# Kernel tuning notes

Measured on AMD Instinct MI355X. Metric: run time of the kernel, lower is better.

The kernel has to match this reference:

```python
import jax, jax.numpy as jnp
import numpy as np

N_NODES = 50000
N_EDGES = 800000
H = 64  # n_hid


def _linear_params(key, fan_in, fan_out):
    lim = 1.0 / np.sqrt(fan_in)
    kw, kb = jax.random.split(key)
    w = jax.random.uniform(kw, (fan_in, fan_out), minval=-lim, maxval=lim, dtype=jnp.float32)
    b = jax.random.uniform(kb, (fan_out,), minval=-lim, maxval=lim, dtype=jnp.float32)
    return w, b


def setup_inputs() -> dict:
    key = jax.random.key(0)
    ks = jax.random.split(key, 10)
    nf_gc = jax.random.normal(ks[0], (N_NODES, H), dtype=jnp.float32)
    src = jax.random.randint(ks[1], (N_EDGES,), 0, N_NODES, dtype=jnp.int32)
    dst = jax.random.randint(ks[2], (N_EDGES,), 0, N_NODES, dtype=jnp.int32)
    res_w1, res_b1 = _linear_params(ks[3], H, H)
    res_w2, res_b2 = _linear_params(ks[4], H, H)
    lin1_w, lin1_b = _linear_params(ks[5], H, H)
    lin2_w, lin2_b = _linear_params(ks[6], H, H)
    msg_w1, msg_b1 = _linear_params(ks[7], 2 * H, 2 * H)
    msg_w2, msg_b2 = _linear_params(ks[8], 2 * H, 2 * H + 1)
    red_w, red_b = _linear_params(ks[9], 3 * H, H)
    return {
        'nf_gc': nf_gc, 'src': src, 'dst': dst,
        'res_w1': res_w1, 'res_b1': res_b1, 'res_w2': res_w2, 'res_b2': res_b2,
        'lin1_w': lin1_w, 'lin1_b': lin1_b, 'lin2_w': lin2_w, 'lin2_b': lin2_b,
        'msg_w1': msg_w1, 'msg_b1': msg_b1, 'msg_w2': msg_w2, 'msg_b2': msg_b2,
        'red_w': red_w, 'red_b': red_b,
    }


def reference(nf_gc, src, dst, res_w1, res_b1, res_w2, res_b2,
              lin1_w, lin1_b, lin2_w, lin2_b,
              msg_w1, msg_b1, msg_w2, msg_b2, red_w, red_b):
    n = nf_gc.shape[0]
    h = lin1_w.shape[0]
    # Residual block: lin2(lin1(x)) + x (no activation)
    x = ((nf_gc @ res_w1 + res_b1) @ res_w2 + res_b2) + nf_gc
    x1 = x @ lin1_w + lin1_b
    # Edge message: concat(src feat, dst feat) -> MLP(2h -> 2h -> 2h+1)
    e = jnp.concatenate([x[src], x[dst]], axis=1)          # [E, 2h]
    hmid = jax.nn.leaky_relu(e @ msg_w1 + msg_b1, 0.2)     # [E, 2h]
    o = hmid @ msg_w2 + msg_b2                             # [E, 2h+1]
    k = jax.nn.sigmoid(o[:, :1])
    f1 = o[:, 1:1 + h] * k
    f2 = o[:, 1 + h:] * k
    # Scatter-reduce: sum for f1, max for f2 (DGL gives 0 for isolated nodes)
    nfoc1 = jax.ops.segment_sum(f1, dst, num_segments=n)
    neg_inf = jnp.array(-jnp.inf, dtype=f2.dtype)
    nfoc2 = jnp.full((n, h), neg_inf, dtype=f2.dtype).at[dst].max(f2)
    deg = jnp.zeros((n,), dtype=f2.dtype).at[dst].add(1.0)
    nfoc2 = jnp.where(deg[:, None] > 0, nfoc2, 0.0)
    # Node reduce MLP (single linear 3h -> h), then outer lin2
    new_x = jnp.concatenate([x, nfoc1, nfoc2], axis=1) @ red_w + red_b
    x2 = new_x @ lin2_w + lin2_b
    return x1 + x2
```

## Files before the change

### kernel.cpp

```cpp
#include <hip/hip_runtime.h>

#define NN 50000
#define NE 800000

typedef _Float16 half8 __attribute__((ext_vector_type(8)));
typedef _Float16 half4 __attribute__((ext_vector_type(4)));
typedef float f32x4 __attribute__((ext_vector_type(4)));
typedef unsigned long long u64;

static const size_t XHOFF  = 0;
static const size_t POFF   = 3200000;
static const size_t QOFF   = 6400000;
static const size_t N1OFF  = 9600000;
static const size_t N2OFF  = 12800000;
static const size_t W2TOFF = 16000000;
static const size_t WGHOFF = 16008192;
static const size_t RW1HOFF= 16008256;
static const size_t RW2HOFF= 16010304;
static const size_t L1WHOFF= 16012352;
static const size_t PWHOFF = 16014400;
static const size_t QWHOFF = 16018496;
static const size_t CNTOFF = 16022592;
static const size_t CUROFF = 16072592;
static const size_t PARTOFF= 16122592;
static const size_t SDOFF  = 16122848;
static const size_t FWOFF  = 17722848;
static const size_t FBOFF  = 17729200;

__device__ __forceinline__ unsigned fenc(float f){
  unsigned b = __float_as_uint(f);
  return (b & 0x80000000u) ? ~b : (b | 0x80000000u);
}
__device__ __forceinline__ float fdec(unsigned u){
  return (u & 0x80000000u) ? __uint_as_float(u & 0x7fffffffu) : __uint_as_float(~u);
}

__device__ __forceinline__ int kperm(int kp){
  const int kg = kp >> 5, rem = kp & 31, kt = rem >> 2, j = rem & 3;
  return kt*16 + kg*4 + j;
}

__global__ __launch_bounds__(256) void prep_k(
    const float* __restrict__ w2, const float* __restrict__ rw1,
    const float* __restrict__ rw2, const float* __restrict__ l1w,
    const float* __restrict__ mw1,
    const float* __restrict__ redw, const float* __restrict__ redb,
    const float* __restrict__ l2w, const float* __restrict__ l2b,
    _Float16* __restrict__ w2t, _Float16* __restrict__ w2gh,
    _Float16* __restrict__ rw1h, _Float16* __restrict__ rw2h,
    _Float16* __restrict__ l1wh, _Float16* __restrict__ pwh,
    _Float16* __restrict__ qwh,
    _Float16* __restrict__ fwh, float* __restrict__ fb,
    const int* __restrict__ dst, unsigned* __restrict__ counts)
{
  __shared__ float sl2[64][8];
  const int b = blockIdx.x;
  if (b < 177){
    int i = b * 256 + threadIdx.x;
    if (i < 16384){
      int c = i >> 7, kp = i & 127;
      w2t[i] = (_Float16)w2[kperm(kp)*129 + 1 + c];
    } else if (i < 16512){
      int kp = i - 16384;
      w2gh[kp] = (_Float16)w2[kperm(kp)*129];
    } else if (i < 20608){
      int idx = i - 16512, c = idx >> 6, k = idx & 63;
      rw1h[idx] = (_Float16)rw1[k*64 + c];
    } else if (i < 24704){
      int idx = i - 20608, c = idx >> 6, k = idx & 63;
      rw2h[idx] = (_Float16)rw2[k*64 + c];
    } else if (i < 28800){
      int idx = i - 24704, c = idx >> 6, k = idx & 63;
      l1wh[idx] = (_Float16)l1w[k*64 + c];
    } else if (i < 36992){
      int idx = i - 28800, c = idx >> 6, k = idx & 63;
      pwh[idx] = (_Float16)mw1[k*128 + c];
    } else if (i < 45184){
      int idx = i - 36992, c = idx >> 6, k = idx & 63;
      qwh[idx] = (_Float16)mw1[(64 + k)*128 + c];
    }
  } else if (b < 185){
    const int b2 = b - 177;
    const int c0 = b2 * 8;
    const int t = threadIdx.x;
    #pragma unroll
    for (int i = 0; i < 2; ++i){
      int idx = t + i*256;
      int j = idx >> 3, cc = idx & 7;
      sl2[j][cc] = l2w[j*64 + c0 + cc];
    }
    __syncthreads();
    for (int o = t; o < 1536; o += 256){
      int k = o >> 3, cc = o & 7;
      const float4* rw = (const float4*)&redw[k*64];
      float a = 0.f;
      #pragma unroll
      for (int q = 0; q < 16; ++q){
        const float4 r4 = rw[q];
        a = fmaf(r4.x, sl2[q*4+0][cc], a);
        a = fmaf(r4.y, sl2[q*4+1][cc], a);
        a = fmaf(r4.z, sl2[q*4+2][cc], a);
        a = fmaf(r4.w, sl2[q*4+3][cc], a);
      }
      fwh[(size_t)(c0 + cc)*192 + k] = (_Float16)a;
    }
    if (t < 8){
      float a = l2b[c0 + t];
      #pragma unroll 8
      for (int j = 0; j < 64; ++j) a = fmaf(redb[j], sl2[j][t], a);
      fb[c0 + t] = a;
    }
  } else {
    int e = (b - 185) * 256 + threadIdx.x;
    if (e < NE) atomicAdd(&counts[dst[e]], 1u);
  }
}

__global__ __launch_bounds__(256) void scanA2(const unsigned* __restrict__ counts,
                                              unsigned* __restrict__ partial,
                                              uint4* __restrict__ nfz)
{
  __shared__ unsigned s[256];
  const int b = blockIdx.x;
  const int t = threadIdx.x;
  if (b < 196){
    const int idx = b * 256 + t;
    s[t] = (idx < NN) ? counts[idx] : 0u;
    __syncthreads();
    for (int d = 128; d > 0; d >>= 1){
      if (t < d) s[t] += s[t + d];
      __syncthreads();
    }
    if (t == 0) partial[b] = s[0];
  } else {
    const size_t i0 = ((size_t)(b - 196) * 256 + t) * 4;
    #pragma unroll
    for (int i = 0; i < 4; ++i){
      const size_t idx = i0 + i;
      if (idx < 1600000) nfz[idx] = make_uint4(0u,0u,0u,0u);
    }
  }
}

__global__ __launch_bounds__(256) void scanC2(const unsigned* __restrict__ counts,
                                              const unsigned* __restrict__ partial,
                                              unsigned* __restrict__ cursor)
{
  __shared__ unsigned sp[256];
  __shared__ unsigned s[256];
  const int t = threadIdx.x;
  const int b = blockIdx.x;
  sp[t] = (t < 196 && t < b) ? partial[t] : 0u;
  __syncthreads();
  for (int d = 128; d > 0; d >>= 1){
    if (t < d) sp[t] += sp[t + d];
    __syncthreads();
  }
  const unsigned boff = sp[0];
  const int idx = b * 256 + t;
  unsigned v = (idx < NN) ? counts[idx] : 0u;
  s[t] = v;
  __syncthreads();
  for (int d = 1; d < 256; d <<= 1){
    unsigned u = (t >= d) ? s[t - d] : 0u;
    __syncthreads();
    s[t] += u;
    __syncthreads();
  }
  if (idx < NN) cursor[idx] = boff + s[t] - v;
}

__global__ __launch_bounds__(256) void combo_k(
    const int* __restrict__ src, const int* __restrict__ dst,
    unsigned* __restrict__ cursor, u64* __restrict__ sdbuf,
    const float* __restrict__ nf,
    const _Float16* __restrict__ rw1h, const float* __restrict__ rb1,
    const _Float16* __restrict__ rw2h, const float* __restrict__ rb2,
    const _Float16* __restrict__ l1wh, const float* __restrict__ l1b,
    const _Float16* __restrict__ pwh, const _Float16* __restrict__ qwh,
    const float* __restrict__ mb1,
    _Float16* __restrict__ xh, _Float16* __restrict__ Pp, _Float16* __restrict__ Qp,
    float* __restrict__ out)
{
  __shared__ _Float16 sM[64][72];
  __shared__ _Float16 sT[64][72];
  const int b = blockIdx.x;
  const int t = threadIdx.x;

  if (b < 3125){
    int e = b * 256 + t;
    if (e < NE){
      const int d = dst[e];
      unsigned slot = atomicAdd(&cursor[d], 1u);
      sdbuf[slot] = ((u64)(unsigned)d << 32) | (unsigned)src[e];
    }
    return;
  }

  const int lane = t & 63, wv = t >> 6;
  const int l15 = lane & 15, kg = lane >> 4;
  const int n0 = (b - 3125) * 64;

  {
    const int rr = t >> 4, c4 = (t & 15) * 4;
    #pragma unroll
    for (int i = 0; i < 4; ++i){
      int r = rr + i*16, n = n0 + r;
      float4 v = make_float4(0.f,0.f,0.f,0.f);
      if (n < NN) v = *(const float4*)&nf[(size_t)n*64 + c4];
      half4 h; h[0]=(_Float16)v.x; h[1]=(_Float16)v.y; h[2]=(_Float16)v.z; h[3]=(_Float16)v.w;
      *(half4*)&sM[r][c4] = h;
    }
  }
  __syncthreads();

  const int col = wv*16 + l15;

  {
    half4 bf[4];
    #pragma unroll
    for (int kt = 0; kt < 4; ++kt) bf[kt] = *(const half4*)&rw1h[col*64 + kt*16 + kg*4];
    const float bias = rb1[col];
    #pragma unroll
    for (int rt = 0; rt < 4; ++rt){
      f32x4 acc = {0.f,0.f,0.f,0.f};
      #pragma unroll
      for (int kt = 0; kt < 4; ++kt){
        const half4 af = *(const half4*)&sM[rt*16 + l15][kt*16 + kg*4];
        acc = __builtin_amdgcn_mfma_f32_16x16x16f16(af, bf[kt], acc, 0, 0, 0);
      }
      #pragma unroll
      for (int reg = 0; reg < 4; ++reg)
        sT[rt*16 + kg*4 + reg][col] = (_Float16)(acc[reg] + bias);
    }
  }
  __syncthreads();

  {
    half4 bf[4];
    #pragma unroll
    for (int kt = 0; kt < 4; ++kt) bf[kt] = *(const half4*)&rw2h[col*64 + kt*16 + kg*4];
    const float bias = rb2[col];
    #pragma unroll
    for (int rt = 0; rt < 4; ++rt){
      f32x4 acc = {0.f,0.f,0.f,0.f};
      #pragma unroll
      for (int kt = 0; kt < 4; ++kt){
        const half4 af = *(const half4*)&sT[rt*16 + l15][kt*16 + kg*4];
        acc = __builtin_amdgcn_mfma_f32_16x16x16f16(af, bf[kt], acc, 0, 0, 0);
      }
      #pragma unroll
      for (int reg = 0; reg < 4; ++reg){
        const int row = rt*16 + kg*4 + reg;
        const float xv = acc[reg] + bias + (float)sM[row][col];
        const _Float16 xvh = (_Float16)xv;
        const int n = n0 + row;
        if (n < NN) xh[(size_t)n*64 + col] = xvh;
        sM[row][col] = xvh;
      }
    }
  }
  __syncthreads();

  {
    half4 bf[4];
    #pragma unroll
    for (int kt = 0; kt < 4; ++kt) bf[kt] = *(const half4*)&l1wh[col*64 + kt*16 + kg*4];
    const float bias = l1b[col];
    #pragma unroll
    for (int rt = 0; rt < 4; ++rt){
      f32x4 acc = {0.f,0.f,0.f,0.f};
      #pragma unroll
      for (int kt = 0; kt < 4; ++kt){
        const half4 af = *(const half4*)&sM[rt*16 + l15][kt*16 + kg*4];
        acc = __builtin_amdgcn_mfma_f32_16x16x16f16(af, bf[kt], acc, 0, 0, 0);
      }
      #pragma unroll
      for (int reg = 0; reg < 4; ++reg){
        const int row = rt*16 + kg*4 + reg;
        const int n = n0 + row;
        if (n < NN) out[(size_t)n*64 + col] = acc[reg] + bias;
      }
    }
  }

  #pragma unroll
  for (int g = 0; g < 2; ++g){
    const _Float16* WH = g ? qwh : pwh;
    _Float16* dstp = g ? Qp : Pp;
    #pragma unroll
    for (int h = 0; h < 2; ++h){
      const int ct = h*4 + wv;
      const int colp = ct*16 + l15;
      half4 bf[4];
      #pragma unroll
      for (int kt = 0; kt < 4; ++kt) bf[kt] = *(const half4*)&WH[colp*64 + kt*16 + kg*4];
      const float bias = g ? 0.f : mb1[colp];
      const int kgc = l15 >> 2, jj = l15 & 3;
      const int pos = kgc*32 + ct*4 + jj;
      #pragma unroll
      for (int rt = 0; rt < 4; ++rt){
        f32x4 acc = {0.f,0.f,0.f,0.f};
        #pragma unroll
        for (int kt = 0; kt < 4; ++kt){
          const half4 af = *(const half4*)&sM[rt*16 + l15][kt*16 + kg*4];
          acc = __builtin_amdgcn_mfma_f32_16x16x16f16(af, bf[kt], acc, 0, 0, 0);
        }
        #pragma unroll
        for (int reg = 0; reg < 4; ++reg){
          const int row = rt*16 + kg*4 + reg;
          const int n = n0 + row;
          if (n < NN) dstp[(size_t)n*128 + pos] = (_Float16)(acc[reg] + bias);
        }
      }
    }
  }
}

__global__ __launch_bounds__(256) void edge_mlp8(
    const u64* __restrict__ sd,
    const _Float16* __restrict__ Pp, const _Float16* __restrict__ Qp,
    const _Float16* __restrict__ w2t, const _Float16* __restrict__ w2gh,
    const float* __restrict__ b2,
    float* __restrict__ nfoc1, unsigned* __restrict__ nfoc2)
{
  __shared__ _Float16 sA[64][136];
  __shared__ _Float16 sOutH[64][136];
  __shared__ float sK[2][64];
  __shared__ int   sD[2][64];
  const int t = threadIdx.x;
  const int lane = t & 63, wv = t >> 6;
  const int r  = lane & 15;
  const int kg = lane >> 4;
  const int row0 = wv * 16;
  const int base = blockIdx.x * 256;

  const int ct0 = wv * 2;
  half4 bf0[8], bf1[8];
  half8 wgr[4];
  float bias0, bias1;
  {
    const int col0 = ct0*16 + r, col1 = (ct0+1)*16 + r;
    bias0 = b2[1 + col0]; bias1 = b2[1 + col1];
    const _Float16* w0p = &w2t[(size_t)col0*128 + kg*32];
    const _Float16* w1p = &w2t[(size_t)col1*128 + kg*32];
    #pragma unroll
    for (int kt = 0; kt < 8; ++kt){
      bf0[kt] = *(const half4*)&w0p[kt*4];
      bf1[kt] = *(const half4*)&w1p[kt*4];
    }
    #pragma unroll
    for (int i = 0; i < 4; ++i) wgr[i] = *(const half8*)&w2gh[kg*32 + i*8];
  }
  const float gb = b2[0];

#define LOADRAW(PH, QH, SS, DD, TILE) { \
    const u64 sdv = sd[base + (TILE)*64 + row0 + r]; \
    SS = (int)(unsigned)(sdv & 0xffffffffu); \
    DD = (int)(unsigned)(sdv >> 32); \
    const _Float16* pr = &Pp[(size_t)SS * 128 + kg*32]; \
    const _Float16* qr = &Qp[(size_t)DD * 128 + kg*32]; \
    PH[0] = *(const half8*)&pr[0];  PH[1] = *(const half8*)&pr[8]; \
    PH[2] = *(const half8*)&pr[16]; PH[3] = *(const half8*)&pr[24]; \
    QH[0] = *(const half8*)&qr[0];  QH[1] = *(const half8*)&qr[8]; \
    QH[2] = *(const half8*)&qr[16]; QH[3] = *(const half8*)&qr[24]; }

#define PROCESS(PH, QH, DD, BUF) { \
    if (kg == 0) sD[BUF][row0 + r] = DD; \
    float gp = 0.f; \
    _Pragma("unroll") \
    for (int i = 0; i < 4; ++i){ \
      half8 mv = PH[i] + QH[i]; \
      const half8 m2 = mv * (_Float16)0.2f; \
      mv = __builtin_elementwise_max(mv, m2); \
      _Pragma("unroll") \
      for (int j = 0; j < 8; ++j) \
        gp = fmaf((float)mv[j], (float)wgr[i][j], gp); \
      *(half8*)&sA[row0 + r][kg*32 + i*8] = mv; \
    } \
    gp += __shfl_xor(gp, 16); \
    gp += __shfl_xor(gp, 32); \
    if (kg == 0) sK[BUF][row0 + r] = 1.f / (1.f + expf(-(gp + gb))); }

#define COMPUTE() { \
    _Pragma("unroll") \
    for (int rt = 0; rt < 4; ++rt){ \
      half4 af[8]; \
      const _Float16* ar = &sA[rt*16 + r][kg*32]; \
      _Pragma("unroll") \
      for (int kt = 0; kt < 8; ++kt) af[kt] = *(const half4*)&ar[kt*4]; \
      f32x4 a0 = {0.f,0.f,0.f,0.f}, a1 = {0.f,0.f,0.f,0.f}; \
      _Pragma("unroll") \
      for (int kt = 0; kt < 8; ++kt){ \
        a0 = __builtin_amdgcn_mfma_f32_16x16x16f16(af[kt], bf0[kt], a0, 0, 0, 0); \
        a1 = __builtin_amdgcn_mfma_f32_16x16x16f16(af[kt], bf1[kt], a1, 0, 0, 0); \
      } \
      _Pragma("unroll") \
      for (int reg = 0; reg < 4; ++reg){ \
        const int row = rt*16 + kg*4 + reg; \
        sOutH[row][ ct0   *16 + r] = (_Float16)(a0[reg] + bias0); \
        sOutH[row][(ct0+1)*16 + r] = (_Float16)(a1[reg] + bias1); \
      } \
    } }

#define REDUCE(BUF) { \
    const int c = t & 127; \
    const int rbeg = (t >> 7) * 32; \
    const bool isSum = c < 64; \
    float acc = isSum ? 0.f : -1e30f; \
    int curd = sD[BUF][rbeg]; \
    _Pragma("unroll 4") \
    for (int rw = rbeg; rw < rbeg + 32; ++rw){ \
      const float v = (float)sOutH[rw][c] * sK[BUF][rw]; \
      acc = isSum ? (acc + v) : fmaxf(acc, v); \
      const bool last = (rw == rbeg + 31) || (sD[BUF][rw + 1] != curd); \
      if (last){ \
        if (isSum){ \
          unsafeAtomicAdd(&nfoc1[(size_t)curd*64 + c], acc); \
          acc = 0.f; \
        } else { \
          atomicMax(&nfoc2[(size_t)curd*64 + (c - 64)], fenc(acc)); \
          acc = -1e30f; \
        } \
        if (rw < rbeg + 31) curd = sD[BUF][rw + 1]; \
      } \
    } }

  int s0, d0, s1, d1;
  half8 ph0[4], qh0[4], ph1[4], qh1[4];

  LOADRAW(ph0, qh0, s0, d0, 0);

  LOADRAW(ph1, qh1, s1, d1, 1);
  PROCESS(ph0, qh0, d0, 0);
  __syncthreads();
  COMPUTE();
  __syncthreads();
  REDUCE(0);

  LOADRAW(ph0, qh0, s0, d0, 2);
  PROCESS(ph1, qh1, d1, 1);
  __syncthreads();
  COMPUTE();
  __syncthreads();
  REDUCE(1);

  LOADRAW(ph1, qh1, s1, d1, 3);
  PROCESS(ph0, qh0, d0, 0);
  __syncthreads();
  COMPUTE();
  __syncthreads();
  REDUCE(0);

  PROCESS(ph1, qh1, d1, 1);
  __syncthreads();
  COMPUTE();
  __syncthreads();
  REDUCE(1);

#undef LOADRAW
#undef PROCESS
#undef COMPUTE
#undef REDUCE
}

__global__ __launch_bounds__(256) void node_post_m(
    const _Float16* __restrict__ xh, const float* __restrict__ nfoc1,
    const unsigned* __restrict__ nfoc2, const unsigned* __restrict__ counts,
    const _Float16* __restrict__ fwh, const float* __restrict__ fb,
    float* __restrict__ out)
{
  __shared__ _Float16 sC[64][200];
  const int t = threadIdx.x;
  const int lane = t & 63, wv = t >> 6;
  const int l15 = lane & 15, kg = lane >> 4;
  const int n0 = blockIdx.x * 64;

  {
    const int rr = t >> 4, c4 = (t & 15) * 4;
    #pragma unroll
    for (int i = 0; i < 4; ++i){
      int r = rr + i*16, n = n0 + r;
      half4 xv = {};
      float4 f1 = make_float4(0,0,0,0);
      uint4 f2 = make_uint4(0,0,0,0);
      bool has = false;
      if (n < NN){
        xv = *(const half4*)&xh[(size_t)n*64 + c4];
        f1 = *(const float4*)&nfoc1[(size_t)n*64 + c4];
        f2 = *(const uint4*)&nfoc2[(size_t)n*64 + c4];
        has = counts[n] > 0u;
      }
      *(half4*)&sC[r][c4] = xv;
      half4 h1; h1[0]=(_Float16)f1.x; h1[1]=(_Float16)f1.y; h1[2]=(_Float16)f1.z; h1[3]=(_Float16)f1.w;
      *(half4*)&sC[r][64 + c4] = h1;
      half4 h2;
      h2[0] = has ? (_Float16)fdec(f2.x) : (_Float16)0.f;
      h2[1] = has ? (_Float16)fdec(f2.y) : (_Float16)0.f;
      h2[2] = has ? (_Float16)fdec(f2.z) : (_Float16)0.f;
      h2[3] = has ? (_Float16)fdec(f2.w) : (_Float16)0.f;
      *(half4*)&sC[r][128 + c4] = h2;
    }
  }
  __syncthreads();

  const int col = wv*16 + l15;
  half4 bf[12];
  #pragma unroll
  for (int kt = 0; kt < 12; ++kt) bf[kt] = *(const half4*)&fwh[col*192 + kt*16 + kg*4];
  const float bias = fb[col];

  #pragma unroll
  for (int rt = 0; rt < 4; ++rt){
    f32x4 acc = {0.f,0.f,0.f,0.f};
    #pragma unroll
    for (int kt = 0; kt < 12; ++kt){
      const half4 af = *(const half4*)&sC[rt*16 + l15][kt*16 + kg*4];
      acc = __builtin_amdgcn_mfma_f32_16x16x16f16(af, bf[kt], acc, 0, 0, 0);
    }
    #pragma unroll
    for (int reg = 0; reg < 4; ++reg){
      const int row = rt*16 + kg*4 + reg;
      const int n = n0 + row;
      if (n < NN) out[(size_t)n*64 + col] += acc[reg] + bias;
    }
  }
}

extern "C" void kernel_launch(void* const* d_in, const int* in_sizes, int n_in,
                              void* d_out, int out_size, void* d_ws, size_t ws_size,
                              hipStream_t stream)
{
  const float* nf   = (const float*)d_in[0];
  const int*   src  = (const int*)d_in[1];
  const int*   dst  = (const int*)d_in[2];
  const float* rw1  = (const float*)d_in[3];
  const float* rb1  = (const float*)d_in[4];
  const float* rw2  = (const float*)d_in[5];
  const float* rb2  = (const float*)d_in[6];
  const float* l1w  = (const float*)d_in[7];
  const float* l1b  = (const float*)d_in[8];
  const float* l2w  = (const float*)d_in[9];
  const float* l2b  = (const float*)d_in[10];
  const float* mw1  = (const float*)d_in[11];
  const float* mb1  = (const float*)d_in[12];
  const float* mw2  = (const float*)d_in[13];
  const float* mb2  = (const float*)d_in[14];
  const float* redw = (const float*)d_in[15];
  const float* redb = (const float*)d_in[16];

  float* ws = (float*)d_ws;
  _Float16*  xh     = (_Float16*)(ws + XHOFF);
  _Float16*  P      = (_Float16*)(ws + POFF);
  _Float16*  Q      = (_Float16*)(ws + QOFF);
  float*     nfoc1  = ws + N1OFF;
  unsigned*  nfoc2  = (unsigned*)(ws + N2OFF);
  _Float16*  w2t    = (_Float16*)(ws + W2TOFF);
  _Float16*  w2gh   = (_Float16*)(ws + WGHOFF);
  _Float16*  rw1h   = (_Float16*)(ws + RW1HOFF);
  _Float16*  rw2h   = (_Float16*)(ws + RW2HOFF);
  _Float16*  l1wh   = (_Float16*)(ws + L1WHOFF);
  _Float16*  pwh    = (_Float16*)(ws + PWHOFF);
  _Float16*  qwh    = (_Float16*)(ws + QWHOFF);
  unsigned*  counts = (unsigned*)(ws + CNTOFF);
  unsigned*  cursor = (unsigned*)(ws + CUROFF);
  unsigned*  partial= (unsigned*)(ws + PARTOFF);
  u64*       sdbuf  = (u64*)(ws + SDOFF);
  _Float16*  fwh    = (_Float16*)(ws + FWOFF);
  float*     fb     = ws + FBOFF;
  float*     out    = (float*)d_out;

  hipMemsetAsync(counts, 0, NN * sizeof(unsigned), stream);
  hipLaunchKernelGGL(prep_k, dim3(185 + 3125), dim3(256), 0, stream,
                     mw2, rw1, rw2, l1w, mw1, redw, redb, l2w, l2b,
                     w2t, w2gh, rw1h, rw2h, l1wh, pwh, qwh, fwh, fb, dst, counts);
  hipLaunchKernelGGL(scanA2, dim3(196 + 1563), dim3(256), 0, stream,
                     counts, partial, (uint4*)nfoc1);
  hipLaunchKernelGGL(scanC2, dim3(196), dim3(256), 0, stream, counts, partial, cursor);
  hipLaunchKernelGGL(combo_k, dim3(3125 + 782), dim3(256), 0, stream,
                     src, dst, cursor, sdbuf,
                     nf, rw1h, rb1, rw2h, rb2, l1wh, l1b, pwh, qwh, mb1,
                     xh, P, Q, out);
  hipLaunchKernelGGL(edge_mlp8, dim3(3125), dim3(256), 0, stream,
                     sdbuf, P, Q, w2t, w2gh, mb2, nfoc1, nfoc2);
  hipLaunchKernelGGL(node_post_m, dim3(782), dim3(256), 0, stream,
                     xh, nfoc1, nfoc2, counts, fwh, fb, out);
}
```

Before: 313.1 us.

## Split edge MLP output into sum/max halves and move zeroing into prep kernel

The edge MLP kernel now computes the f1 (sum) and f2 (max) output halves in two passes through a half-width shared buffer. The sum and max reductions become separate uniform loops with no per-row sum-or-max branch, and each thread handles 16 rows instead of 32. This reduces shared memory per block, which may allow more resident blocks, but adds two extra barriers per tile. Separately, zeroing of nfoc1 moves from the scan kernel into the prep kernel, so scanA only does the block partial sums.

```diff
diff --git a/kernel.cpp b/kernel.cpp
--- a/kernel.cpp
+++ b/kernel.cpp
@@ -51,6 +51,7 @@
     _Float16* __restrict__ l1wh, _Float16* __restrict__ pwh,
     _Float16* __restrict__ qwh,
     _Float16* __restrict__ fwh, float* __restrict__ fb,
+    uint4* __restrict__ nfz,
     const int* __restrict__ dst, unsigned* __restrict__ counts)
 {
   __shared__ float sl2[64][8];
@@ -110,36 +111,32 @@
       for (int j = 0; j < 64; ++j) a = fmaf(redb[j], sl2[j][t], a);
       fb[c0 + t] = a;
     }
-  } else {
-    int e = (b - 185) * 256 + threadIdx.x;
-    if (e < NE) atomicAdd(&counts[dst[e]], 1u);
-  }
-}
-
-__global__ __launch_bounds__(256) void scanA2(const unsigned* __restrict__ counts,
-                                              unsigned* __restrict__ partial,
-                                              uint4* __restrict__ nfz)
-{
-  __shared__ unsigned s[256];
-  const int b = blockIdx.x;
-  const int t = threadIdx.x;
-  if (b < 196){
-    const int idx = b * 256 + t;
-    s[t] = (idx < NN) ? counts[idx] : 0u;
-    __syncthreads();
-    for (int d = 128; d > 0; d >>= 1){
-      if (t < d) s[t] += s[t + d];
-      __syncthreads();
-    }
-    if (t == 0) partial[b] = s[0];
-  } else {
-    const size_t i0 = ((size_t)(b - 196) * 256 + t) * 4;
+  } else if (b < 1748){
+    const size_t i0 = ((size_t)(b - 185) * 256 + threadIdx.x) * 4;
     #pragma unroll
     for (int i = 0; i < 4; ++i){
       const size_t idx = i0 + i;
       if (idx < 1600000) nfz[idx] = make_uint4(0u,0u,0u,0u);
     }
-  }
+  } else {
+    int e = (b - 1748) * 256 + threadIdx.x;
+    if (e < NE) atomicAdd(&counts[dst[e]], 1u);
+  }
+}
+
+__global__ __launch_bounds__(256) void scanA(const unsigned* __restrict__ counts,
+                                             unsigned* __restrict__ partial)
+{
+  __shared__ unsigned s[256];
+  const int t = threadIdx.x;
+  const int idx = blockIdx.x * 256 + t;
+  s[t] = (idx < NN) ? counts[idx] : 0u;
+  __syncthreads();
+  for (int d = 128; d > 0; d >>= 1){
+    if (t < d) s[t] += s[t + d];
+    __syncthreads();
+  }
+  if (t == 0) partial[blockIdx.x] = s[0];
 }
 
 __global__ __launch_bounds__(256) void scanC2(const unsigned* __restrict__ counts,
@@ -317,7 +314,7 @@
   }
 }
 
-__global__ __launch_bounds__(256) void edge_mlp8(
+__global__ __launch_bounds__(256) void edge_mlp10(
     const u64* __restrict__ sd,
     const _Float16* __restrict__ Pp, const _Float16* __restrict__ Qp,
     const _Float16* __restrict__ w2t, const _Float16* __restrict__ w2gh,
@@ -325,7 +322,7 @@
     float* __restrict__ nfoc1, unsigned* __restrict__ nfoc2)
 {
   __shared__ _Float16 sA[64][136];
-  __shared__ _Float16 sOutH[64][136];
+  __shared__ _Float16 sOutHh[64][72];
   __shared__ float sK[2][64];
   __shared__ int   sD[2][64];
   const int t = threadIdx.x;
@@ -335,12 +332,11 @@
   const int row0 = wv * 16;
   const int base = blockIdx.x * 256;
 
-  const int ct0 = wv * 2;
   half4 bf0[8], bf1[8];
   half8 wgr[4];
   float bias0, bias1;
   {
-    const int col0 = ct0*16 + r, col1 = (ct0+1)*16 + r;
+    const int col0 = wv*16 + r, col1 = (wv+4)*16 + r;
     bias0 = b2[1 + col0]; bias1 = b2[1 + col1];
     const _Float16* w0p = &w2t[(size_t)col0*128 + kg*32];
     const _Float16* w1p = &w2t[(size_t)col1*128 + kg*32];
@@ -382,50 +378,66 @@
     gp += __shfl_xor(gp, 32); \
     if (kg == 0) sK[BUF][row0 + r] = 1.f / (1.f + expf(-(gp + gb))); }
 
-#define COMPUTE() { \
+#define COMPUTE_HALF(BF, BIAS) { \
     _Pragma("unroll") \
     for (int rt = 0; rt < 4; ++rt){ \
       half4 af[8]; \
       const _Float16* ar = &sA[rt*16 + r][kg*32]; \
       _Pragma("unroll") \
       for (int kt = 0; kt < 8; ++kt) af[kt] = *(const half4*)&ar[kt*4]; \
-      f32x4 a0 = {0.f,0.f,0.f,0.f}, a1 = {0.f,0.f,0.f,0.f}; \
+      f32x4 a0 = {0.f,0.f,0.f,0.f}; \
       _Pragma("unroll") \
-      for (int kt = 0; kt < 8; ++kt){ \
-        a0 = __builtin_amdgcn_mfma_f32_16x16x16f16(af[kt], bf0[kt], a0, 0, 0, 0); \
-        a1 = __builtin_amdgcn_mfma_f32_16x16x16f16(af[kt], bf1[kt], a1, 0, 0, 0); \
-      } \
+      for (int kt = 0; kt < 8; ++kt) \
+        a0 = __builtin_amdgcn_mfma_f32_16x16x16f16(af[kt], BF[kt], a0, 0, 0, 0); \
       _Pragma("unroll") \
       for (int reg = 0; reg < 4; ++reg){ \
         const int row = rt*16 + kg*4 + reg; \
-        sOutH[row][ ct0   *16 + r] = (_Float16)(a0[reg] + bias0); \
-        sOutH[row][(ct0+1)*16 + r] = (_Float16)(a1[reg] + bias1); \
+        sOutHh[row][wv*16 + r] = (_Float16)(a0[reg] + BIAS); \
       } \
     } }
 
-#define REDUCE(BUF) { \
-    const int c = t & 127; \
-    const int rbeg = (t >> 7) * 32; \
-    const bool isSum = c < 64; \
-    float acc = isSum ? 0.f : -1e30f; \
+#define REDUCE_SUM(BUF) { \
+    const int c = t & 63; \
+    const int rbeg = (t >> 6) * 16; \
+    float acc = 0.f; \
     int curd = sD[BUF][rbeg]; \
     _Pragma("unroll 4") \
-    for (int rw = rbeg; rw < rbeg + 32; ++rw){ \
-      const float v = (float)sOutH[rw][c] * sK[BUF][rw]; \
-      acc = isSum ? (acc + v) : fmaxf(acc, v); \
-      const bool last = (rw == rbeg + 31) || (sD[BUF][rw + 1] != curd); \
+    for (int rw = rbeg; rw < rbeg + 16; ++rw){ \
+      acc += (float)sOutHh[rw][c] * sK[BUF][rw]; \
+      const bool last = (rw == rbeg + 15) || (sD[BUF][rw + 1] != curd); \
       if (last){ \
-        if (isSum){ \
-          unsafeAtomicAdd(&nfoc1[(size_t)curd*64 + c], acc); \
-          acc = 0.f; \
-        } else { \
-          atomicMax(&nfoc2[(size_t)curd*64 + (c - 64)], fenc(acc)); \
-          acc = -1e30f; \
-        } \
-        if (rw < rbeg + 31) curd = sD[BUF][rw + 1]; \
+        unsafeAtomicAdd(&nfoc1[(size_t)curd*64 + c], acc); \
+        acc = 0.f; \
+        if (rw < rbeg + 15) curd = sD[BUF][rw + 1]; \
       } \
     } }
 
+#define REDUCE_MAX(BUF) { \
+    const int c = t & 63; \
+    const int rbeg = (t >> 6) * 16; \
+    float acc = -1e30f; \
+    int curd = sD[BUF][rbeg]; \
+    _Pragma("unroll 4") \
+    for (int rw = rbeg; rw < rbeg + 16; ++rw){ \
+      acc = fmaxf(acc, (float)sOutHh[rw][c] * sK[BUF][rw]); \
+      const bool last = (rw == rbeg + 15) || (sD[BUF][rw + 1] != curd); \
+      if (last){ \
+        atomicMax(&nfoc2[(size_t)curd*64 + c], fenc(acc)); \
+        acc = -1e30f; \
+        if (rw < rbeg + 15) curd = sD[BUF][rw + 1]; \
+      } \
+    } }
+
+#define TILE_BODY(BUF) \
+    __syncthreads(); \
+    COMPUTE_HALF(bf0, bias0); \
+    __syncthreads(); \
+    REDUCE_SUM(BUF); \
+    __syncthreads(); \
+    COMPUTE_HALF(bf1, bias1); \
+    __syncthreads(); \
+    REDUCE_MAX(BUF);
+
   int s0, d0, s1, d1;
   half8 ph0[4], qh0[4], ph1[4], qh1[4];
 
@@ -433,35 +445,25 @@
 
   LOADRAW(ph1, qh1, s1, d1, 1);
   PROCESS(ph0, qh0, d0, 0);
-  __syncthreads();
-  COMPUTE();
-  __syncthreads();
-  REDUCE(0);
+  TILE_BODY(0);
 
   LOADRAW(ph0, qh0, s0, d0, 2);
   PROCESS(ph1, qh1, d1, 1);
-  __syncthreads();
-  COMPUTE();
-  __syncthreads();
-  REDUCE(1);
+  TILE_BODY(1);
 
   LOADRAW(ph1, qh1, s1, d1, 3);
   PROCESS(ph0, qh0, d0, 0);
-  __syncthreads();
-  COMPUTE();
-  __syncthreads();
-  REDUCE(0);
+  TILE_BODY(0);
 
   PROCESS(ph1, qh1, d1, 1);
-  __syncthreads();
-  COMPUTE();
-  __syncthreads();
-  REDUCE(1);
+  TILE_BODY(1);
 
 #undef LOADRAW
 #undef PROCESS
-#undef COMPUTE
-#undef REDUCE
+#undef COMPUTE_HALF
+#undef REDUCE_SUM
+#undef REDUCE_MAX
+#undef TILE_BODY
 }
 
 __global__ __launch_bounds__(256) void node_post_m(
@@ -571,17 +573,17 @@
   float*     out    = (float*)d_out;
 
   hipMemsetAsync(counts, 0, NN * sizeof(unsigned), stream);
-  hipLaunchKernelGGL(prep_k, dim3(185 + 3125), dim3(256), 0, stream,
+  hipLaunchKernelGGL(prep_k, dim3(1748 + 3125), dim3(256), 0, stream,
                      mw2, rw1, rw2, l1w, mw1, redw, redb, l2w, l2b,
-                     w2t, w2gh, rw1h, rw2h, l1wh, pwh, qwh, fwh, fb, dst, counts);
-  hipLaunchKernelGGL(scanA2, dim3(196 + 1563), dim3(256), 0, stream,
-                     counts, partial, (uint4*)nfoc1);
+                     w2t, w2gh, rw1h, rw2h, l1wh, pwh, qwh, fwh, fb,
+                     (uint4*)nfoc1, dst, counts);
+  hipLaunchKernelGGL(scanA, dim3(196), dim3(256), 0, stream, counts, partial);
   hipLaunchKernelGGL(scanC2, dim3(196), dim3(256), 0, stream, counts, partial, cursor);
   hipLaunchKernelGGL(combo_k, dim3(3125 + 782), dim3(256), 0, stream,
                      src, dst, cursor, sdbuf,
                      nf, rw1h, rb1, rw2h, rb2, l1wh, l1b, pwh, qwh, mb1,
                      xh, P, Q, out);
-  hipLaunchKernelGGL(edge_mlp8, dim3(3125), dim3(256), 0, stream,
+  hipLaunchKernelGGL(edge_mlp10, dim3(3125), dim3(256), 0, stream,
                      sdbuf, P, Q, w2t, w2gh, mb2, nfoc1, nfoc2);
   hipLaunchKernelGGL(node_post_m, dim3(782), dim3(256), 0, stream,
                      xh, nfoc1, nfoc2, counts, fwh, fb, out);
```

Measured after the change: 278.2 us. 1.13x faster.
